# Performance work log

Hardware: AMD Instinct MI355X
Metric: run time of the kernel (lower is better)

Reference implementation:

```python
import jax, jax.numpy as jnp
import numpy as np

B, N, F, P, HID, OUT = 4, 20000, 8, 12, 64, 1
E = 320000


def _glorot(k, shape):
    lim = float(np.sqrt(6.0 / (shape[0] + shape[1])))
    return jax.random.uniform(k, shape, jnp.float32, -lim, lim)


def setup_inputs() -> dict:
    key = jax.random.key(0)
    ks = jax.random.split(key, 20)
    inp = {
        "x": jax.random.normal(ks[0], (B, N, F, P), jnp.float32),
        "edge_index": jax.random.randint(ks[1], (2, E), 0, N, jnp.int64),
        "edge_attr": jax.random.uniform(ks[2], (E,), jnp.float32),
        # GCNConv weights (stored [in, out]) + biases for z, r, h gates
        "conv_z_w": _glorot(ks[3], (F, HID)), "conv_z_b": jnp.zeros((HID,), jnp.float32),
        "conv_r_w": _glorot(ks[4], (F, HID)), "conv_r_b": jnp.zeros((HID,), jnp.float32),
        "conv_h_w": _glorot(ks[5], (F, HID)), "conv_h_b": jnp.zeros((HID,), jnp.float32),
        # GRU linear layers on cat([conv_out, H]) -> HID (stored [in, out])
        "lin_z_w": _glorot(ks[6], (2 * HID, HID)), "lin_z_b": jnp.zeros((HID,), jnp.float32),
        "lin_r_w": _glorot(ks[7], (2 * HID, HID)), "lin_r_b": jnp.zeros((HID,), jnp.float32),
        "lin_h_w": _glorot(ks[8], (2 * HID, HID)), "lin_h_b": jnp.zeros((HID,), jnp.float32),
        # temporal attention logits over periods
        "attention": jax.random.uniform(ks[9], (P,), jnp.float32),
        # final linear: HID -> OUT*P
        "out_w": _glorot(ks[10], (HID, OUT * P)), "out_b": jnp.zeros((OUT * P,), jnp.float32),
    }
    return inp


def reference(x, edge_index, edge_attr,
              conv_z_w, conv_z_b, conv_r_w, conv_r_b, conv_h_w, conv_h_b,
              lin_z_w, lin_z_b, lin_r_w, lin_r_b, lin_h_w, lin_h_b,
              attention, out_w, out_b):
    Bb, Nn, Ff, Pp = x.shape
    Hh = conv_z_w.shape[1]

    # GCN normalization with self loops: A_hat = D^-1/2 (A + I) D^-1/2
    loop = jnp.arange(Nn)
    row = jnp.concatenate([edge_index[0], loop])
    col = jnp.concatenate([edge_index[1], loop])
    w = jnp.concatenate([edge_attr, jnp.ones((Nn,), x.dtype)])
    deg = jax.ops.segment_sum(w, col, num_segments=Nn)
    dinv = jnp.where(deg > 0, jax.lax.rsqrt(deg), 0.0)
    norm = dinv[row] * w * dinv[col]  # [E+N]

    def gcn(xt, W, b):
        # xt: [B, N, F] -> [B, N, H]
        xw = jnp.einsum('bnf,fh->bnh', xt, W)
        msg = xw[:, row, :] * norm[None, :, None]            # gather over source nodes
        agg = jax.vmap(lambda m: jax.ops.segment_sum(m, col, num_segments=Nn))(msg)
        return agg + b

    H0 = jnp.zeros((Bb, Nn, Hh), x.dtype)  # A3TGCN2 passes H=None each period -> zeros

    def tgcn_cell(xt):
        Z = jax.nn.sigmoid(jnp.concatenate([gcn(xt, conv_z_w, conv_z_b), H0], -1) @ lin_z_w + lin_z_b)
        R = jax.nn.sigmoid(jnp.concatenate([gcn(xt, conv_r_w, conv_r_b), H0], -1) @ lin_r_w + lin_r_b)
        Ht = jnp.tanh(jnp.concatenate([gcn(xt, conv_h_w, conv_h_b), H0 * R], -1) @ lin_h_w + lin_h_b)
        return Z * H0 + (1.0 - Z) * Ht

    probs = jax.nn.softmax(attention)
    xs = jnp.moveaxis(x, -1, 0)  # [P, B, N, F]

    def step(acc, inp):
        xt, p = inp
        return acc + p * tgcn_cell(xt), None

    h_accum, _ = jax.lax.scan(step, jnp.zeros((Bb, Nn, Hh), x.dtype), (xs, probs))

    h = jax.nn.relu(h_accum)
    out = h @ out_w + out_b                 # [B, N, OUT*P]
    return out.reshape(Bb, Nn, -1, Pp)      # [B, N, OUT, P]
```

## Files before the change

### kernel.cpp

```cpp
#include <hip/hip_runtime.h>

#define NN 20000
#define EE 320000
#define CAP 64
#define SVC 72
#define OVCAP 8192
#define EBLK 313

#define WZ_O 0
#define BZ_O 512
#define WH_O 576
#define BH_O 1088
#define OWT_O 1152
#define OB_O 1968
#define PR_O 1980
#define NCONST 1992

__device__ __forceinline__ float b2f(unsigned short h) {
  union { unsigned int u; float f; } v; v.u = ((unsigned int)h) << 16; return v.f;
}
__device__ __forceinline__ unsigned short f2b(float f) {
  union { unsigned int u; float f; } v; v.f = f;
  unsigned int u = v.u;
  unsigned int r = (u + 0x7fffu + ((u >> 16) & 1u)) >> 16;
  return (unsigned short)r;
}
__device__ __forceinline__ float ldw(const void* p, int i, int isbf) {
  return isbf ? b2f(((const unsigned short*)p)[i]) : ((const float*)p)[i];
}
__device__ __forceinline__ void upk(unsigned int w, float& x0, float& x1) {
  union { unsigned int u; float f; } lo, hi;
  lo.u = w << 16; hi.u = w & 0xffff0000u;
  x0 = lo.f; x1 = hi.f;
}
__device__ __forceinline__ float degf(unsigned long long dc) {
  return (float)(unsigned int)dc * (1.0f / 1048576.0f);
}

__global__ void __launch_bounds__(256) k_append(
    const void* __restrict__ ei, const void* __restrict__ ea,
    unsigned long long* __restrict__ degcnt,
    unsigned int* __restrict__ slab,
    int* __restrict__ ovf_cnt, int* __restrict__ ovf_dst,
    unsigned int* __restrict__ ovf_pack, float* __restrict__ consts,
    const void* czw, const void* czb, const void* chw, const void* chb,
    const void* lzw, const void* lzb, const void* lhw, const void* lhb,
    const void* att, const void* ow, const void* ob) {
  __shared__ int sfl[2];
  const int tid = threadIdx.x;
  if (tid < 64) {
    unsigned long long b1 = __ballot((((const unsigned int*)ea)[tid] >> 15) & 1u);
    unsigned long long b2 = __ballot(((const unsigned int*)ei)[2 * tid + 1] != 0u);
    if (tid == 0) {
      sfl[0] = (b1 == 0ull) ? 1 : 0;
      sfl[1] = (b2 == 0ull) ? 1 : 0;
    }
  }
  __syncthreads();
  const int isbf = sfl[0], is64 = sfl[1];

  if (blockIdx.x == EBLK) {
    for (int idx = tid; idx < 512; idx += 256) {
      int f = idx >> 6, k = idx & 63;
      float sz = 0.f, sh = 0.f;
      for (int h = 0; h < 64; ++h) {
        sz += ldw(czw, f * 64 + h, isbf) * ldw(lzw, h * 64 + k, isbf);
        sh += ldw(chw, f * 64 + h, isbf) * ldw(lhw, h * 64 + k, isbf);
      }
      consts[WZ_O + idx] = sz; consts[WH_O + idx] = sh;
    }
    for (int idx = tid; idx < 64; idx += 256) {
      float sz = ldw(lzb, idx, isbf), sh = ldw(lhb, idx, isbf);
      for (int h = 0; h < 64; ++h) {
        sz += ldw(czb, h, isbf) * ldw(lzw, h * 64 + idx, isbf);
        sh += ldw(chb, h, isbf) * ldw(lhw, h * 64 + idx, isbf);
      }
      consts[BZ_O + idx] = sz; consts[BH_O + idx] = sh;
    }
    for (int idx = tid; idx < 816; idx += 256) {
      int p = idx / 68, kk = idx % 68;
      consts[OWT_O + idx] = (kk < 64) ? ldw(ow, kk * 12 + p, isbf) : 0.f;
    }
    if (tid < 12) consts[OB_O + tid] = ldw(ob, tid, isbf);
    if (tid == 0) {
      float a[12]; float m = -1e30f;
      for (int p = 0; p < 12; ++p) { a[p] = ldw(att, p, isbf); m = fmaxf(m, a[p]); }
      float ssum = 0.f;
      for (int p = 0; p < 12; ++p) { a[p] = __expf(a[p] - m); ssum += a[p]; }
      for (int p = 0; p < 12; ++p) consts[PR_O + p] = a[p] / ssum;
    }
    return;
  }

  const int e0 = blockIdx.x * 1024 + tid;
#pragma unroll
  for (int u = 0; u < 4; ++u) {
    int e = e0 + 256 * u;
    if (e >= EE) continue;
    int r, c;
    if (is64) {
      r = (int)((const unsigned int*)ei)[2 * e];
      c = (int)((const unsigned int*)ei)[2 * (EE + e)];
    } else {
      r = ((const int*)ei)[e];
      c = ((const int*)ei)[EE + e];
    }
    unsigned short wb;
    float w;
    if (isbf) { wb = ((const unsigned short*)ea)[e]; w = b2f(wb); }
    else      { w = ((const float*)ea)[e]; wb = f2b(w); }
    unsigned long long pk = (1ull << 32) |
        (unsigned long long)(unsigned int)__float2int_rn(w * 1048576.0f);
    unsigned long long old = atomicAdd(&degcnt[c], pk);
    int pos = (int)(old >> 32);
    unsigned int packed = ((unsigned int)wb << 16) | (unsigned int)r;
    if (pos < CAP) {
      slab[c * CAP + pos] = packed;
    } else {
      int oi = atomicAdd(ovf_cnt, 1);
      if (oi < OVCAP) { ovf_dst[oi] = c; ovf_pack[oi] = packed; }
    }
  }
}

#define ACC8(u, v)                                           \
  { float x0, x1;                                            \
    upk((u).x, x0, x1); a[0] += (v) * x0; a[1] += (v) * x1;  \
    upk((u).y, x0, x1); a[2] += (v) * x0; a[3] += (v) * x1;  \
    upk((u).z, x0, x1); a[4] += (v) * x0; a[5] += (v) * x1;  \
    upk((u).w, x0, x1); a[6] += (v) * x0; a[7] += (v) * x1; }

#define ACCF8(u0, u1, v)                                                       \
  { a[0] += (v) * (u0).x; a[1] += (v) * (u0).y; a[2] += (v) * (u0).z;          \
    a[3] += (v) * (u0).w; a[4] += (v) * (u1).x; a[5] += (v) * (u1).y;          \
    a[6] += (v) * (u1).z; a[7] += (v) * (u1).w; }

__global__ void __launch_bounds__(256) k_node(
    const void* __restrict__ x, const void* __restrict__ ea,
    const unsigned long long* __restrict__ degcnt,
    const unsigned int* __restrict__ slab,
    const int* __restrict__ ovf_cnt, const int* __restrict__ ovf_dst,
    const unsigned int* __restrict__ ovf_pack,
    const float* __restrict__ consts,
    void* __restrict__ out) {
  __shared__ __align__(16) float sow[840];
  __shared__ __align__(16) int2  sv[4 * SVC];
  __shared__ __align__(16) float accT[4 * 384];
  __shared__ __align__(16) float hw[4 * 272];
  __shared__ int swcnt[4];
  __shared__ int sfl[1];

  const int tid  = threadIdx.x;
  const int w    = tid >> 6;
  const int lane = tid & 63;
  const int n    = blockIdx.x * 4 + w;

  if (tid < 64) {
    unsigned long long b1 = __ballot((((const unsigned int*)ea)[tid] >> 15) & 1u);
    if (tid == 0) sfl[0] = (b1 == 0ull) ? 1 : 0;
  }
  for (int i = tid; i < 840; i += 256) sow[i] = consts[OWT_O + i];
  float wz[8], wh[8];
#pragma unroll
  for (int f = 0; f < 8; ++f) {
    wz[f] = consts[WZ_O + f * 64 + lane];
    wh[f] = consts[WH_O + f * 64 + lane];
  }
  const float bz = consts[BZ_O + lane], bh = consts[BH_O + lane];
  __syncthreads();
  const int isbf = sfl[0];

  unsigned long long dcn = degcnt[n];
  int cnt = (int)(dcn >> 32);
  int base = cnt < CAP ? cnt : CAP;
  const float dn = rsqrtf(degf(dcn) + 1.0f);
  int2* svw = &sv[w * SVC];
  if (lane == 0) swcnt[w] = base;
  if (lane < base) {
    unsigned int pk = slab[n * CAP + lane];
    int s = (int)(pk & 0xffffu);
    float v = b2f((unsigned short)(pk >> 16)) * rsqrtf(degf(degcnt[s]) + 1.0f);
    svw[lane] = make_int2(s * 96, __float_as_int(v));
  }
  int m0 = base;
  {
    int ov = ovf_cnt[0];
    if (ov > 0) {
      if (ov > OVCAP) ov = OVCAP;
      for (int i = lane; i < ov; i += 64) {
        if (ovf_dst[i] == n) {
          int idx = atomicAdd(&swcnt[w], 1);
          if (idx < SVC - 1) {
            unsigned int pk = ovf_pack[i];
            int s = (int)(pk & 0xffffu);
            float v = b2f((unsigned short)(pk >> 16)) *
                      rsqrtf(degf(degcnt[s]) + 1.0f);
            svw[idx] = make_int2(s * 96, __float_as_int(v));
          }
        }
      }
      __builtin_amdgcn_wave_barrier();
      m0 = swcnt[w];
      if (m0 > SVC - 1) m0 = SVC - 1;
    }
  }
  if (lane == 0) svw[m0] = make_int2(n * 96, __float_as_int(dn));
  const int m1 = m0 + 1;
  __builtin_amdgcn_wave_barrier();

  float a[8];
#pragma unroll
  for (int t = 0; t < 8; ++t) a[t] = 0.f;
  if (lane < 48) {
    const long xbase = (long)(lane / 12) * (NN * 96) + 8 * (lane % 12);
    if (isbf) {
      const unsigned short* xb = (const unsigned short*)x;
      int j = 0;
      for (; j + 1 < m1; j += 2) {
        int2 e0 = svw[j], e1 = svw[j + 1];
        uint4 u0 = *(const uint4*)(xb + xbase + e0.x);
        uint4 u1 = *(const uint4*)(xb + xbase + e1.x);
        float v0 = __int_as_float(e0.y), v1 = __int_as_float(e1.y);
        ACC8(u0, v0); ACC8(u1, v1);
      }
      if (j < m1) {
        int2 e0 = svw[j];
        uint4 u0 = *(const uint4*)(xb + xbase + e0.x);
        float v0 = __int_as_float(e0.y);
        ACC8(u0, v0);
      }
    } else {
      const float* xf = (const float*)x;
      int j = 0;
      for (; j + 1 < m1; j += 2) {
        int2 e0 = svw[j], e1 = svw[j + 1];
        const float4* p0 = (const float4*)(xf + xbase + e0.x);
        const float4* p1 = (const float4*)(xf + xbase + e1.x);
        float4 u00 = p0[0], u01 = p0[1], u10 = p1[0], u11 = p1[1];
        float v0 = __int_as_float(e0.y), v1 = __int_as_float(e1.y);
        ACCF8(u00, u01, v0); ACCF8(u10, u11, v1);
      }
      if (j < m1) {
        int2 e0 = svw[j];
        const float4* p0 = (const float4*)(xf + xbase + e0.x);
        float4 u00 = p0[0], u01 = p0[1];
        float v0 = __int_as_float(e0.y);
        ACCF8(u00, u01, v0);
      }
    }
    float* accTw = &accT[w * 384];
    const int bq = (lane / 12) * 96, oc = 8 * (lane % 12);
#pragma unroll
    for (int t = 0; t < 8; ++t) {
      int eib = oc + t;
      int f = eib / 12, p = eib % 12;
      accTw[bq + p * 8 + f] = dn * a[t];
    }
  }
  __builtin_amdgcn_wave_barrier();

  {
    const float* accTw = &accT[w * 384];
    float* hww = &hw[w * 272];
#pragma unroll
    for (int b = 0; b < 4; ++b) {
      float hbl = 0.f;
#pragma unroll
      for (int p = 0; p < 12; ++p) {
        const float4* A = (const float4*)&accTw[b * 96 + p * 8];
        float4 A0 = A[0], A1 = A[1];
        float za = bz + A0.x * wz[0] + A0.y * wz[1] + A0.z * wz[2] + A0.w * wz[3]
                      + A1.x * wz[4] + A1.y * wz[5] + A1.z * wz[6] + A1.w * wz[7];
        float ta = bh + A0.x * wh[0] + A0.y * wh[1] + A0.z * wh[2] + A0.w * wh[3]
                      + A1.x * wh[4] + A1.y * wh[5] + A1.z * wh[6] + A1.w * wh[7];
        float ea2 = __expf(za);
        float eh = __expf(2.0f * fminf(ta, 40.0f));
        hbl += sow[828 + p] * (eh - 1.0f) *
               __builtin_amdgcn_rcpf((1.0f + ea2) * (1.0f + eh));
      }
      hww[b * 68 + lane] = fmaxf(hbl, 0.f);
    }
  }
  __builtin_amdgcn_wave_barrier();

  if (lane < 48) {
    const float* hww = &hw[w * 272];
    int b = lane / 12, p = lane % 12;
    float o = sow[816 + p];
#pragma unroll
    for (int kq = 0; kq < 16; ++kq) {
      float4 hv = *(const float4*)&hww[b * 68 + 4 * kq];
      float4 wv = *(const float4*)&sow[p * 68 + 4 * kq];
      o += hv.x * wv.x + hv.y * wv.y + hv.z * wv.z + hv.w * wv.w;
    }
    int oi = (b * NN + n) * 12 + p;
    if (isbf) ((unsigned short*)out)[oi] = f2b(o);
    else      ((float*)out)[oi] = o;
  }
}

extern "C" void kernel_launch(void* const* d_in, const int* in_sizes, int n_in,
                              void* d_out, int out_size, void* d_ws, size_t ws_size,
                              hipStream_t stream) {
  const void* x   = d_in[0];
  const void* ei  = d_in[1];
  const void* ea  = d_in[2];
  const void* czw = d_in[3];
  const void* czb = d_in[4];
  const void* chw = d_in[7];
  const void* chb = d_in[8];
  const void* lzw = d_in[9];
  const void* lzb = d_in[10];
  const void* lhw = d_in[13];
  const void* lhb = d_in[14];
  const void* att = d_in[15];
  const void* ow  = d_in[16];
  const void* ob  = d_in[17];

  char* ws = (char*)d_ws;
  float* consts  = (float*)(ws + 256);
  unsigned long long* degcnt = (unsigned long long*)(ws + 8448);
  int*   ovf_cnt = (int*)  (ws + 168448);
  int*   ovf_dst = (int*)  (ws + 168704);
  unsigned int* ovf_pack = (unsigned int*)(ws + 201472);
  unsigned int* slab     = (unsigned int*)(ws + 234240);

  hipMemsetAsync(ws + 8448, 0, 160064, stream);
  k_append<<<dim3(EBLK + 1), dim3(256), 0, stream>>>(ei, ea, degcnt, slab,
                                                     ovf_cnt, ovf_dst, ovf_pack,
                                                     consts,
                                                     czw, czb, chw, chb,
                                                     lzw, lzb, lhw, lhb,
                                                     att, ow, ob);
  k_node<<<dim3(NN / 4), dim3(256), 0, stream>>>(x, ea, degcnt, slab,
                                                 ovf_cnt, ovf_dst, ovf_pack,
                                                 consts, d_out);
}
```

Measured before the change: 232.5 us.

## Spread gather over all 64 lanes with 6-wide chunks and fold exp scales into weights

The neighbour-gather loop now uses all 64 lanes of each wave (16 lanes per batch, 6 features each) instead of 48 lanes doing 8 each. Edge weights are premultiplied by the destination's inverse-sqrt degree, so the final scaling is dropped. The log2(e) factors are folded into the precomputed gate weights so the gates can use exp2 directly, and the attention probabilities are hoisted into registers. This gives more lanes in flight per node, at the cost of narrower, less aligned 12-byte and float2 loads and a modified accT transpose layout.

```diff
diff --git a/kernel.cpp b/kernel.cpp
--- a/kernel.cpp
+++ b/kernel.cpp
@@ -16,6 +16,8 @@
 #define PR_O 1980
 #define NCONST 1992
 
+#define LOG2E 1.44269504088896340736f
+
 __device__ __forceinline__ float b2f(unsigned short h) {
   union { unsigned int u; float f; } v; v.u = ((unsigned int)h) << 16; return v.f;
 }
@@ -36,6 +38,15 @@
 __device__ __forceinline__ float degf(unsigned long long dc) {
   return (float)(unsigned int)dc * (1.0f / 1048576.0f);
 }
+__device__ __forceinline__ float ex2(float x) {
+#if __has_builtin(__builtin_amdgcn_exp2f)
+  return __builtin_amdgcn_exp2f(x);
+#else
+  return __exp2f(x);
+#endif
+}
+
+struct __align__(4) U3 { unsigned int x, y, z; };
 
 __global__ void __launch_bounds__(256) k_append(
     const void* __restrict__ ei, const void* __restrict__ ea,
@@ -67,7 +78,8 @@
         sz += ldw(czw, f * 64 + h, isbf) * ldw(lzw, h * 64 + k, isbf);
         sh += ldw(chw, f * 64 + h, isbf) * ldw(lhw, h * 64 + k, isbf);
       }
-      consts[WZ_O + idx] = sz; consts[WH_O + idx] = sh;
+      consts[WZ_O + idx] = sz * LOG2E;
+      consts[WH_O + idx] = sh * (2.0f * LOG2E);
     }
     for (int idx = tid; idx < 64; idx += 256) {
       float sz = ldw(lzb, idx, isbf), sh = ldw(lhb, idx, isbf);
@@ -75,7 +87,8 @@
         sz += ldw(czb, h, isbf) * ldw(lzw, h * 64 + idx, isbf);
         sh += ldw(chb, h, isbf) * ldw(lhw, h * 64 + idx, isbf);
       }
-      consts[BZ_O + idx] = sz; consts[BH_O + idx] = sh;
+      consts[BZ_O + idx] = sz * LOG2E;
+      consts[BH_O + idx] = sh * (2.0f * LOG2E);
     }
     for (int idx = tid; idx < 816; idx += 256) {
       int p = idx / 68, kk = idx % 68;
@@ -123,17 +136,15 @@
   }
 }
 
-#define ACC8(u, v)                                           \
+#define ACC6(u, v)                                           \
   { float x0, x1;                                            \
     upk((u).x, x0, x1); a[0] += (v) * x0; a[1] += (v) * x1;  \
     upk((u).y, x0, x1); a[2] += (v) * x0; a[3] += (v) * x1;  \
-    upk((u).z, x0, x1); a[4] += (v) * x0; a[5] += (v) * x1;  \
-    upk((u).w, x0, x1); a[6] += (v) * x0; a[7] += (v) * x1; }
-
-#define ACCF8(u0, u1, v)                                                       \
-  { a[0] += (v) * (u0).x; a[1] += (v) * (u0).y; a[2] += (v) * (u0).z;          \
-    a[3] += (v) * (u0).w; a[4] += (v) * (u1).x; a[5] += (v) * (u1).y;          \
-    a[6] += (v) * (u1).z; a[7] += (v) * (u1).w; }
+    upk((u).z, x0, x1); a[4] += (v) * x0; a[5] += (v) * x1; }
+
+#define ACCF6(f0, f1, f2, v)                                                   \
+  { a[0] += (v) * (f0).x; a[1] += (v) * (f0).y; a[2] += (v) * (f1).x;          \
+    a[3] += (v) * (f1).y; a[4] += (v) * (f2).x; a[5] += (v) * (f2).y; }
 
 __global__ void __launch_bounds__(256) k_node(
     const void* __restrict__ x, const void* __restrict__ ea,
@@ -179,7 +190,7 @@
   if (lane < base) {
     unsigned int pk = slab[n * CAP + lane];
     int s = (int)(pk & 0xffffu);
-    float v = b2f((unsigned short)(pk >> 16)) * rsqrtf(degf(degcnt[s]) + 1.0f);
+    float v = b2f((unsigned short)(pk >> 16)) * rsqrtf(degf(degcnt[s]) + 1.0f) * dn;
     svw[lane] = make_int2(s * 96, __float_as_int(v));
   }
   int m0 = base;
@@ -194,7 +205,7 @@
             unsigned int pk = ovf_pack[i];
             int s = (int)(pk & 0xffffu);
             float v = b2f((unsigned short)(pk >> 16)) *
-                      rsqrtf(degf(degcnt[s]) + 1.0f);
+                      rsqrtf(degf(degcnt[s]) + 1.0f) * dn;
             svw[idx] = make_int2(s * 96, __float_as_int(v));
           }
         }
@@ -204,64 +215,64 @@
       if (m0 > SVC - 1) m0 = SVC - 1;
     }
   }
-  if (lane == 0) svw[m0] = make_int2(n * 96, __float_as_int(dn));
+  if (lane == 0) svw[m0] = make_int2(n * 96, __float_as_int(dn * dn));
   const int m1 = m0 + 1;
   __builtin_amdgcn_wave_barrier();
 
-  float a[8];
-#pragma unroll
-  for (int t = 0; t < 8; ++t) a[t] = 0.f;
-  if (lane < 48) {
-    const long xbase = (long)(lane / 12) * (NN * 96) + 8 * (lane % 12);
+  float a[6];
+#pragma unroll
+  for (int t = 0; t < 6; ++t) a[t] = 0.f;
+  {
+    const int i15 = lane & 15;
+    const long xbase = (long)(lane >> 4) * (NN * 96) + 6 * i15;
     if (isbf) {
-      const unsigned short* xb = (const unsigned short*)x;
+      const unsigned short* xr = (const unsigned short*)x + xbase;
       int j = 0;
       for (; j + 1 < m1; j += 2) {
         int2 e0 = svw[j], e1 = svw[j + 1];
-        uint4 u0 = *(const uint4*)(xb + xbase + e0.x);
-        uint4 u1 = *(const uint4*)(xb + xbase + e1.x);
+        U3 u0 = *(const U3*)(xr + e0.x);
+        U3 u1 = *(const U3*)(xr + e1.x);
         float v0 = __int_as_float(e0.y), v1 = __int_as_float(e1.y);
-        ACC8(u0, v0); ACC8(u1, v1);
+        ACC6(u0, v0); ACC6(u1, v1);
       }
       if (j < m1) {
         int2 e0 = svw[j];
-        uint4 u0 = *(const uint4*)(xb + xbase + e0.x);
+        U3 u0 = *(const U3*)(xr + e0.x);
         float v0 = __int_as_float(e0.y);
-        ACC8(u0, v0);
+        ACC6(u0, v0);
       }
     } else {
-      const float* xf = (const float*)x;
+      const float* xf = (const float*)x + xbase;
       int j = 0;
       for (; j + 1 < m1; j += 2) {
         int2 e0 = svw[j], e1 = svw[j + 1];
-        const float4* p0 = (const float4*)(xf + xbase + e0.x);
-        const float4* p1 = (const float4*)(xf + xbase + e1.x);
-        float4 u00 = p0[0], u01 = p0[1], u10 = p1[0], u11 = p1[1];
+        const float2* p0 = (const float2*)(xf + e0.x);
+        const float2* p1 = (const float2*)(xf + e1.x);
+        float2 u00 = p0[0], u01 = p0[1], u02 = p0[2];
+        float2 u10 = p1[0], u11 = p1[1], u12 = p1[2];
         float v0 = __int_as_float(e0.y), v1 = __int_as_float(e1.y);
-        ACCF8(u00, u01, v0); ACCF8(u10, u11, v1);
+        ACCF6(u00, u01, u02, v0); ACCF6(u10, u11, u12, v1);
       }
       if (j < m1) {
         int2 e0 = svw[j];
-        const float4* p0 = (const float4*)(xf + xbase + e0.x);
-        float4 u00 = p0[0], u01 = p0[1];
+        const float2* p0 = (const float2*)(xf + e0.x);
+        float2 u00 = p0[0], u01 = p0[1], u02 = p0[2];
         float v0 = __int_as_float(e0.y);
-        ACCF8(u00, u01, v0);
-      }
-    }
-    float* accTw = &accT[w * 384];
-    const int bq = (lane / 12) * 96, oc = 8 * (lane % 12);
-#pragma unroll
-    for (int t = 0; t < 8; ++t) {
-      int eib = oc + t;
-      int f = eib / 12, p = eib % 12;
-      accTw[bq + p * 8 + f] = dn * a[t];
-    }
+        ACCF6(u00, u01, u02, v0);
+      }
+    }
+    float* aw = &accT[w * 384 + (lane >> 4) * 96 + (i15 & 1) * 48 + (i15 >> 1)];
+#pragma unroll
+    for (int t = 0; t < 6; ++t) aw[8 * t] = a[t];
   }
   __builtin_amdgcn_wave_barrier();
 
   {
     const float* accTw = &accT[w * 384];
     float* hww = &hw[w * 272];
+    float prv[12];
+#pragma unroll
+    for (int p = 0; p < 12; ++p) prv[p] = sow[828 + p];
 #pragma unroll
     for (int b = 0; b < 4; ++b) {
       float hbl = 0.f;
@@ -273,10 +284,11 @@
                       + A1.x * wz[4] + A1.y * wz[5] + A1.z * wz[6] + A1.w * wz[7];
         float ta = bh + A0.x * wh[0] + A0.y * wh[1] + A0.z * wh[2] + A0.w * wh[3]
                       + A1.x * wh[4] + A1.y * wh[5] + A1.z * wh[6] + A1.w * wh[7];
-        float ea2 = __expf(za);
-        float eh = __expf(2.0f * fminf(ta, 40.0f));
-        hbl += sow[828 + p] * (eh - 1.0f) *
-               __builtin_amdgcn_rcpf((1.0f + ea2) * (1.0f + eh));
+        float ea2 = ex2(za);
+        float eh = ex2(fminf(ta, 115.0f));
+        float num = eh - 1.0f;
+        float den = (1.0f + ea2) * (1.0f + eh);
+        hbl += prv[p] * (num * __builtin_amdgcn_rcpf(den));
       }
       hww[b * 68 + lane] = fmaxf(hbl, 0.f);
     }
```

Result: no change. 230.8 us (-0.7%).
